# Kernel tuning notes

Measured on AMD Instinct MI355X. Metric: run time of the kernel, lower is better.

Reference implementation:

```python
import jax, jax.numpy as jnp
import numpy as np

# dims
B, A, CIN, CC = 512, 256, 7, 16          # batch, num_actions, input channels, conv channels
D, H, DH, E = 48, 8, 6, 512              # token_dimension, heads, head_dim, num_embeddings
S, T = 32, 32                            # num_input_tokens, num_output_tokens
AH = H * DH                              # 48
NL = 4                                   # attention layers
CONV_IN = A * CC                         # 4096
ENC = S * D                              # 1536
DEC_OUT = A * CIN                        # 1792
SCALE = float(np.sqrt(D))                # module uses sqrt(input_embedding_dim)
EPS = 1e-5


def _ln(x, g, b):
    m = jnp.mean(x, axis=-1, keepdims=True)
    v = jnp.var(x, axis=-1, keepdims=True)
    return (x - m) * jax.lax.rsqrt(v + EPS) * g + b


def setup_inputs() -> dict:
    key = jax.random.key(0)
    ks = iter(jax.random.split(key, 64))
    def rn(shape, s=0.05):
        return jax.random.normal(next(ks), shape, dtype=jnp.float32) * s
    inp = {}
    inp['x'] = jax.random.normal(next(ks), (B, A, CIN), dtype=jnp.float32)
    inp['u'] = jax.random.uniform(next(ks), (T, B), dtype=jnp.float32)
    inp['bn_g'] = jnp.ones((CIN,), jnp.float32); inp['bn_b'] = jnp.zeros((CIN,), jnp.float32)
    inp['conv_w'] = rn((CC, CIN, 5)); inp['conv_b'] = jnp.zeros((CC,), jnp.float32)
    inp['tk_W1'] = rn((CONV_IN, 2 * CONV_IN)); inp['tk_b1'] = jnp.zeros((2 * CONV_IN,), jnp.float32)
    inp['tk_W2'] = rn((2 * CONV_IN, ENC)); inp['tk_b2'] = jnp.zeros((ENC,), jnp.float32)
    for nm in ('q', 'k', 'v'):
        inp['ln%s_g' % nm] = jnp.ones((NL, D), jnp.float32)
        inp['ln%s_b' % nm] = jnp.zeros((NL, D), jnp.float32)
        inp['W%s' % nm] = rn((NL, D, AH))
        inp['b%s' % nm] = jnp.zeros((NL, AH), jnp.float32)
    inp['Wo'] = rn((NL, AH, D)); inp['bo'] = jnp.zeros((NL, D), jnp.float32)
    inp['mln_g'] = jnp.ones((NL, D), jnp.float32); inp['mln_b'] = jnp.zeros((NL, D), jnp.float32)
    inp['W1'] = rn((NL, D, 2 * D)); inp['b1'] = jnp.zeros((NL, 2 * D), jnp.float32)
    inp['W2'] = rn((NL, 2 * D, D)); inp['b2'] = jnp.zeros((NL, D), jnp.float32)
    inp['emb'] = rn((D, E), 1.0)          # nn.Parameter(torch.randn(D, E))
    inp['pos_enc'] = rn((T, D), 1.0)      # nn.Parameter(torch.randn(T, D))
    inp['dec_W1'] = rn((ENC, 2 * ENC)); inp['dec_b1'] = jnp.zeros((2 * ENC,), jnp.float32)
    inp['dec_W2'] = rn((2 * ENC, DEC_OUT)); inp['dec_b2'] = jnp.zeros((DEC_OUT,), jnp.float32)
    return inp


def _fwd(x, u, bn_g, bn_b, conv_w, conv_b, tk_W1, tk_b1, tk_W2, tk_b2,
         lnq_g, lnq_b, Wq, bq, lnk_g, lnk_b, Wk, bk, lnv_g, lnv_b, Wv, bv, Wo, bo,
         mln_g, mln_b, W1, b1, W2, b2, emb, pos_enc, dec_W1, dec_b1, dec_W2, dec_b2):
    # --- conv stem (BatchNorm1d in training mode: batch statistics) ---
    xt = x.transpose(0, 2, 1)                              # [B, 7, A]
    mu = jnp.mean(xt, axis=(0, 2), keepdims=True)
    var = jnp.var(xt, axis=(0, 2), keepdims=True)
    xn = (xt - mu) * jax.lax.rsqrt(var + EPS) * bn_g[None, :, None] + bn_b[None, :, None]
    xc = jax.lax.conv_general_dilated(xn, conv_w, (1,), ((2, 2),),
                                      dimension_numbers=('NCH', 'OIH', 'NCH')) + conv_b[None, :, None]
    xf = xc.reshape(B, -1)                                 # [B, 16*A]
    h = jax.nn.relu(xf @ tk_W1 + tk_b1)
    toks = (h @ tk_W2 + tk_b2).reshape(B, S, D)            # [B, S, D]

    STOT = S + T
    kc = jnp.zeros((NL, B, H, STOT, DH), jnp.float32)
    vc = jnp.zeros_like(kc)

    # --- prefill pass (output discarded; fills KV caches) ---
    ii = jnp.arange(S)[:, None]; jj = jnp.arange(S)[None, :]
    pre_mask = jnp.where(jj - ii >= S - 1, -999.0, 0.0)    # triu(-999, diagonal=S-1), as in source
    xcur = toks
    for l in range(NL):
        q = (_ln(xcur, lnq_g[l], lnq_b[l]) @ Wq[l] + bq[l]).reshape(B, S, H, DH).transpose(0, 2, 1, 3)
        k = (_ln(xcur, lnk_g[l], lnk_b[l]) @ Wk[l] + bk[l]).reshape(B, S, H, DH).transpose(0, 2, 1, 3)
        v = (_ln(xcur, lnv_g[l], lnv_b[l]) @ Wv[l] + bv[l]).reshape(B, S, H, DH).transpose(0, 2, 1, 3)
        kc = kc.at[l, :, :, :S].set(k)
        vc = vc.at[l, :, :, :S].set(v)
        attn = jax.nn.softmax(jnp.einsum('bhqd,bhkd->bhqk', q, k) / SCALE + pre_mask, axis=-1)
        o = jnp.einsum('bhqk,bhkd->bhqd', attn, v).transpose(0, 2, 1, 3).reshape(B, S, AH)
        xcur = o @ Wo[l] + bo[l] + xcur
        hh = jax.nn.relu(_ln(xcur, mln_g[l], mln_b[l]) @ W1[l] + b1[l])
        xcur = hh @ W2[l] + b2[l]

    jidx = jnp.arange(STOT)

    def step(carry, xs):
        kc, vc = carry
        i, pe, uu = xs
        p = S + i                                          # cache length before this step
        xtk = jnp.broadcast_to(pe, (B, 1, D))
        newk, newv = [], []
        for l in range(NL):
            q = (_ln(xtk, lnq_g[l], lnq_b[l]) @ Wq[l] + bq[l]).reshape(B, 1, H, DH).transpose(0, 2, 1, 3)
            k = (_ln(xtk, lnk_g[l], lnk_b[l]) @ Wk[l] + bk[l]).reshape(B, 1, H, DH).transpose(0, 2, 1, 3)
            v = (_ln(xtk, lnv_g[l], lnv_b[l]) @ Wv[l] + bv[l]).reshape(B, 1, H, DH).transpose(0, 2, 1, 3)
            kcl = jax.lax.dynamic_update_slice(kc[l], k, (0, 0, p, 0))
            vcl = jax.lax.dynamic_update_slice(vc[l], v, (0, 0, p, 0))
            scores = jnp.einsum('bhqd,bhkd->bhqk', q, kcl) / SCALE
            # source mask: -999 added for positions >= mask_offset (includes the new token itself)
            scores = scores + jnp.where(jidx >= p, -999.0, 0.0)
            attn = jax.nn.softmax(scores, axis=-1)
            o = jnp.einsum('bhqk,bhkd->bhqd', attn, vcl).transpose(0, 2, 1, 3).reshape(B, 1, AH)
            xtk = o @ Wo[l] + bo[l] + xtk
            hh = jax.nn.relu(_ln(xtk, mln_g[l], mln_b[l]) @ W1[l] + b1[l])
            xtk = hh @ W2[l] + b2[l]
            newk.append(kcl); newv.append(vcl)
        attended = xtk                                     # [B, 1, D]
        probs = jax.nn.softmax((attended @ emb).reshape(B, E), axis=1)
        cdf = jnp.cumsum(probs, axis=1)
        idx = jnp.clip(jnp.sum((cdf < uu[:, None]).astype(jnp.int32), axis=1), 0, E - 1)
        sel = emb.T[idx].reshape(B, 1, D)
        st = sel + attended - jax.lax.stop_gradient(attended)  # straight-through
        return (jnp.stack(newk), jnp.stack(newv)), st

    (_, _), outs = jax.lax.scan(step, (kc, vc), (jnp.arange(T), pos_enc, u))
    out_tokens = outs.transpose(1, 0, 2, 3).reshape(B, T * D)
    dh_ = jax.nn.relu(out_tokens @ dec_W1 + dec_b1)
    traj = (dh_ @ dec_W2 + dec_b2).reshape(B, A, CIN)
    return traj


def reference(x, u, bn_g, bn_b, conv_w, conv_b, tk_W1, tk_b1, tk_W2, tk_b2,
              lnq_g, lnq_b, Wq, bq, lnk_g, lnk_b, Wk, bk, lnv_g, lnv_b, Wv, bv, Wo, bo,
              mln_g, mln_b, W1, b1, W2, b2, emb, pos_enc, dec_W1, dec_b1, dec_W2, dec_b2):
    return _fwd(x, u, bn_g, bn_b, conv_w, conv_b, tk_W1, tk_b1, tk_W2, tk_b2,
                lnq_g, lnq_b, Wq, bq, lnk_g, lnk_b, Wk, bk, lnv_g, lnv_b, Wv, bv, Wo, bo,
                mln_g, mln_b, W1, b1, W2, b2, emb, pos_enc, dec_W1, dec_b1, dec_W2, dec_b2)
```

## Files before the change

kernel.cpp:

```cpp
#include <hip/hip_runtime.h>

static const double SCALE_ = 6.928203230275509;

__device__ inline float  fma_t(float a, float b, float c)  { return fmaf(a, b, c); }
__device__ inline double fma_t(double a, double b, double c){ return fma(a, b, c); }

__device__ __attribute__((noinline)) double dotW(const double* a,
                                                 const float* W, int n, int ldw,
                                                 double init) {
  double a0 = init, a1 = 0.0;
#pragma unroll 2
  for (int i = 0; i < n; i += 2) {
    a0 = fma(a[i],     (double)W[i * ldw],       a0);
    a1 = fma(a[i + 1], (double)W[(i + 1) * ldw], a1);
  }
  return a0 + a1;
}

__device__ __forceinline__ double dot48_row(const double* a, const float* Wrow, double init) {
  double c0 = init, c1 = 0.0, c2 = 0.0, c3 = 0.0;
#pragma unroll
  for (int i = 0; i < 48; i += 4) {
    const float4 wv = *(const float4*)(Wrow + i);
    c0 = fma(a[i],     (double)wv.x, c0);
    c1 = fma(a[i + 1], (double)wv.y, c1);
    c2 = fma(a[i + 2], (double)wv.z, c2);
    c3 = fma(a[i + 3], (double)wv.w, c3);
  }
  return (c0 + c1) + (c2 + c3);
}

__device__ __forceinline__ double dot96_row(const double* a, const float* Wrow, double init) {
  double c0 = init, c1 = 0.0, c2 = 0.0, c3 = 0.0;
#pragma unroll
  for (int i = 0; i < 96; i += 4) {
    const float4 wv = *(const float4*)(Wrow + i);
    c0 = fma(a[i],     (double)wv.x, c0);
    c1 = fma(a[i + 1], (double)wv.y, c1);
    c2 = fma(a[i + 2], (double)wv.z, c2);
    c3 = fma(a[i + 3], (double)wv.w, c3);
  }
  return (c0 + c1) + (c2 + c3);
}

__device__ __attribute__((noinline)) double2 ln_stats48(const double* x) {
  double s0 = 0, s1 = 0, q0 = 0, q1 = 0;
#pragma unroll 2
  for (int i = 0; i < 48; i += 2) {
    const double va = x[i], vb = x[i + 1];
    s0 += va; q0 = fma(va, va, q0);
    s1 += vb; q1 = fma(vb, vb, q1);
  }
  const double m = (s0 + s1) / 48.0;
  const double rs = 1.0 / sqrt((q0 + q1) / 48.0 - m * m + 1e-5);
  return make_double2(m, rs);
}

__device__ __attribute__((noinline)) double exp_ni(double x) { return exp(x); }

__global__ __launch_bounds__(256) void bn_partial_kernel(const float* __restrict__ x,
                                                         double* __restrict__ part) {
  __shared__ double sh[256 * 14];
  const int tid = threadIdx.x;
  const int idx = blockIdx.x * 256 + tid;
  const float* p = x + (size_t)idx * 7;
  for (int c = 0; c < 7; ++c) {
    double v = (double)p[c];
    sh[tid * 14 + c] = v;
    sh[tid * 14 + 7 + c] = v * v;
  }
  __syncthreads();
  if (tid < 14) {
    double acc = 0.0;
    for (int t = 0; t < 256; ++t) acc += sh[t * 14 + tid];
    part[blockIdx.x * 14 + tid] = acc;
  }
}

__global__ void bn_final_kernel(const double* __restrict__ part,
                                const float* __restrict__ g, const float* __restrict__ bb,
                                double* __restrict__ stat) {
  const int c = threadIdx.x;
  if (c < 7) {
    double s = 0.0, s2 = 0.0;
    for (int i = 0; i < 512; ++i) { s += part[i * 14 + c]; s2 += part[i * 14 + 7 + c]; }
    const double mean = s / 131072.0;
    const double var = s2 / 131072.0 - mean * mean;
    const double rstd = 1.0 / sqrt(var + 1e-5);
    const double scale = rstd * (double)g[c];
    stat[c] = scale;
    stat[7 + c] = (double)bb[c] - mean * scale;
  }
}

__global__ __launch_bounds__(256) void conv_kernel(const float* __restrict__ x,
                                                   const float* __restrict__ wconv,
                                                   const float* __restrict__ cb,
                                                   const double* __restrict__ stat,
                                                   double* __restrict__ xf) {
  __shared__ double wsh[560 + 14];
  const int tid = threadIdx.x;
  for (int i = tid; i < 560; i += 256) wsh[i] = (double)wconv[i];
  for (int i = tid; i < 14; i += 256) wsh[560 + i] = stat[i];
  __syncthreads();
  const int idx = blockIdx.x * 256 + tid;
  const int a = idx & 255;
  const int o = (idx >> 8) & 15;
  const int b = idx >> 12;
  double acc = (double)cb[o];
  const float* xb = x + (size_t)b * (256 * 7);
  for (int k = 0; k < 5; ++k) {
    const int pos = a + k - 2;
    if (pos < 0 || pos >= 256) continue;
    const float* xp = xb + pos * 7;
    for (int ci = 0; ci < 7; ++ci) {
      const double xn = (double)xp[ci] * wsh[560 + ci] + wsh[567 + ci];
      acc = fma(xn, wsh[(o * 7 + ci) * 5 + k], acc);
    }
  }
  xf[idx] = acc;
}

template <typename T, bool BIAS, bool RELU>
__global__ __launch_bounds__(256) void gemm128_kernel(const T* __restrict__ A,
                                                      const float* __restrict__ Bm,
                                                      const float* __restrict__ bias,
                                                      T* __restrict__ C,
                                                      const int M, const int N, const int K,
                                                      const int kc) {
  __shared__ T As[16][130];
  __shared__ T Bs[16][66];
  const int tid = threadIdx.x;
  const int tx = tid & 15, ty = tid >> 4;
  const int n0 = blockIdx.x * 64, m0 = blockIdx.y * 128;
  const int k0 = blockIdx.z * kc, kend = k0 + kc;
  const int ar = tid >> 1, ac = (tid & 1) * 8;
  const int br = tid >> 4, bc = (tid & 15) * 4;
  const T* Ap = A + (size_t)(m0 + ar) * K;
  const float* Bp = Bm + (size_t)br * N + n0 + bc;
  T acc[8][4] = {};
  for (int k = k0; k < kend; k += 16) {
    T av8[8];
#pragma unroll
    for (int i = 0; i < 8; ++i) av8[i] = Ap[k + ac + i];
    const float4 bw = *(const float4*)(Bp + (size_t)k * N);
#pragma unroll
    for (int i = 0; i < 8; ++i) As[ac + i][ar] = av8[i];
    Bs[br][bc] = (T)bw.x; Bs[br][bc + 1] = (T)bw.y;
    Bs[br][bc + 2] = (T)bw.z; Bs[br][bc + 3] = (T)bw.w;
    __syncthreads();
#pragma unroll
    for (int kk = 0; kk < 16; ++kk) {
      T a[8], b[4];
#pragma unroll
      for (int i = 0; i < 8; ++i) a[i] = As[kk][ty * 8 + i];
#pragma unroll
      for (int j = 0; j < 4; ++j) b[j] = Bs[kk][tx * 4 + j];
#pragma unroll
      for (int i = 0; i < 8; ++i)
#pragma unroll
        for (int j = 0; j < 4; ++j) acc[i][j] = fma_t(a[i], b[j], acc[i][j]);
    }
    __syncthreads();
  }
  T* Cp = C + (size_t)blockIdx.z * M * N;
#pragma unroll
  for (int i = 0; i < 8; ++i) {
    const int row = m0 + ty * 8 + i;
#pragma unroll
    for (int j = 0; j < 4; ++j) {
      const int col = n0 + tx * 4 + j;
      T v = acc[i][j];
      if (BIAS) v += (T)bias[col];
      if (RELU) v = v > (T)0 ? v : (T)0;
      Cp[(size_t)row * N + col] = v;
    }
  }
}

template <typename T, bool BIAS, bool RELU>
__global__ __launch_bounds__(256) void gemm_kernel(const T* __restrict__ A,
                                                   const float* __restrict__ Bm,
                                                   const float* __restrict__ bias,
                                                   T* __restrict__ C,
                                                   const int M, const int N, const int K,
                                                   const int kc) {
  __shared__ T As[16][65];
  __shared__ T Bs[16][65];
  const int tid = threadIdx.x;
  const int tx = tid & 15, ty = tid >> 4;
  const int n0 = blockIdx.x * 64, m0 = blockIdx.y * 64;
  const int k0 = blockIdx.z * kc, kend = k0 + kc;
  const int ar = tid >> 2, ac = (tid & 3) * 4;
  const int br = tid >> 4, bc = (tid & 15) * 4;
  const T* Ap = A + (size_t)(m0 + ar) * K;
  const float* Bp = Bm + (size_t)br * N + n0 + bc;
  T acc[4][4] = {};
  for (int k = k0; k < kend; k += 16) {
    const T a0 = Ap[k + ac], a1 = Ap[k + ac + 1], a2 = Ap[k + ac + 2], a3 = Ap[k + ac + 3];
    const float4 bw = *(const float4*)(Bp + (size_t)k * N);
    As[ac][ar] = a0; As[ac + 1][ar] = a1; As[ac + 2][ar] = a2; As[ac + 3][ar] = a3;
    Bs[br][bc] = (T)bw.x; Bs[br][bc + 1] = (T)bw.y; Bs[br][bc + 2] = (T)bw.z; Bs[br][bc + 3] = (T)bw.w;
    __syncthreads();
#pragma unroll
    for (int kk = 0; kk < 16; ++kk) {
      T av[4], bv2[4];
#pragma unroll
      for (int i = 0; i < 4; ++i) av[i] = As[kk][ty * 4 + i];
#pragma unroll
      for (int j = 0; j < 4; ++j) bv2[j] = Bs[kk][tx * 4 + j];
#pragma unroll
      for (int i = 0; i < 4; ++i)
#pragma unroll
        for (int j = 0; j < 4; ++j) acc[i][j] = fma_t(av[i], bv2[j], acc[i][j]);
    }
    __syncthreads();
  }
  T* Cp = C + (size_t)blockIdx.z * M * N;
#pragma unroll
  for (int i = 0; i < 4; ++i) {
    const int row = m0 + ty * 4 + i;
#pragma unroll
    for (int j = 0; j < 4; ++j) {
      const int col = n0 + tx * 4 + j;
      T v = acc[i][j];
      if (BIAS) v += (T)bias[col];
      if (RELU) v = v > (T)0 ? v : (T)0;
      Cp[(size_t)row * N + col] = v;
    }
  }
}

__global__ __launch_bounds__(256) void reduce2_bias_kernel(const double* __restrict__ part,
                                                           const float* __restrict__ bias,
                                                           double* __restrict__ out,
                                                           const int MN, const int N) {
  const int i = blockIdx.x * 256 + threadIdx.x;
  if (i < MN) out[i] = part[i] + part[MN + i] + (double)bias[i % N];
}

__global__ __launch_bounds__(256) void transpose_weights_kernel(
    const float* __restrict__ Wq, const float* __restrict__ Wk,
    const float* __restrict__ Wv, const float* __restrict__ Wo,
    const float* __restrict__ W1, const float* __restrict__ W2,
    const float* __restrict__ emb,
    float* __restrict__ WqT, float* __restrict__ WkT,
    float* __restrict__ WvT, float* __restrict__ WoT,
    float* __restrict__ W1T, float* __restrict__ W2T,
    float* __restrict__ embT) {
  const int t = blockIdx.x * 256 + threadIdx.x;
  if (t < 36864) {
    const int a = t / 9216, r = t - a * 9216;
    const int l = r / 2304, e = r - l * 2304;
    const int i = e / 48, j = e - i * 48;
    const float* src = a == 0 ? Wq : a == 1 ? Wk : a == 2 ? Wv : Wo;
    float* dst = a == 0 ? WqT : a == 1 ? WkT : a == 2 ? WvT : WoT;
    dst[l * 2304 + j * 48 + i] = src[l * 2304 + i * 48 + j];
  } else if (t < 55296) {
    const int t1 = t - 36864;
    const int l = t1 / 4608, e = t1 - l * 4608;
    const int i = e / 96, j = e - i * 96;
    W1T[l * 4608 + j * 48 + i] = W1[l * 4608 + i * 96 + j];
  } else if (t < 73728) {
    const int t2 = t - 55296;
    const int l = t2 / 4608, e = t2 - l * 4608;
    const int i = e / 48, j = e - i * 48;
    W2T[l * 4608 + j * 96 + i] = W2[l * 4608 + i * 48 + j];
  } else {
    const int t3 = t - 73728;
    const int d = t3 / 512, e = t3 - d * 512;
    embT[e * 48 + d] = emb[d * 512 + e];
  }
}

__global__ __launch_bounds__(256) void prefill_kernel(
    const double* __restrict__ toks,
    const float* __restrict__ lnq_g, const float* __restrict__ lnq_b,
    const float* __restrict__ Wq, const float* __restrict__ bq,
    const float* __restrict__ lnk_g, const float* __restrict__ lnk_b,
    const float* __restrict__ Wk, const float* __restrict__ bk,
    const float* __restrict__ lnv_g, const float* __restrict__ lnv_b,
    const float* __restrict__ Wv, const float* __restrict__ bvv,
    const float* __restrict__ Wo, const float* __restrict__ bo,
    const float* __restrict__ mln_g, const float* __restrict__ mln_b,
    const float* __restrict__ W1, const float* __restrict__ b1,
    const float* __restrict__ W2, const float* __restrict__ b2,
    double* __restrict__ kcache, double* __restrict__ vcache) {
  const int b = blockIdx.x, tid = threadIdx.x;
  __shared__ double xcur[1536], abuf[1536], qbuf[1536], kvbuf[3072];
  __shared__ double mean[32], rstd[32];
  double* kb = kvbuf;
  double* vb = kvbuf + 1536;

#pragma unroll 1
  for (int i = tid; i < 1536; i += 256) xcur[i] = toks[(size_t)b * 1536 + i];
  __syncthreads();

#pragma unroll 1
  for (int l = 0; l < 4; ++l) {
    if (tid < 32) {
      double s = 0.0, s2 = 0.0;
#pragma unroll 4
      for (int i = 0; i < 48; ++i) { const double v = xcur[tid * 48 + i]; s += v; s2 += v * v; }
      const double m = s / 48.0;
      mean[tid] = m;
      rstd[tid] = 1.0 / sqrt(s2 / 48.0 - m * m + 1e-5);
    }
    __syncthreads();
    const bool last = (l == 3);

    if (!last) {
#pragma unroll 1
      for (int i = tid; i < 1536; i += 256) {
        const int t = i / 48, d = i % 48;
        abuf[i] = (xcur[i] - mean[t]) * rstd[t] * (double)lnq_g[l * 48 + d] + (double)lnq_b[l * 48 + d];
      }
      __syncthreads();
#pragma unroll 1
      for (int i = tid; i < 1536; i += 256) {
        const int t = i / 48, j = i % 48;
        qbuf[i] = dotW(abuf + t * 48, Wq + l * 2304 + j, 48, 48, (double)bq[l * 48 + j]);
      }
      __syncthreads();
    }
#pragma unroll 1
    for (int i = tid; i < 1536; i += 256) {
      const int t = i / 48, d = i % 48;
      abuf[i] = (xcur[i] - mean[t]) * rstd[t] * (double)lnk_g[l * 48 + d] + (double)lnk_b[l * 48 + d];
    }
    __syncthreads();
#pragma unroll 1
    for (int i = tid; i < 1536; i += 256) {
      const int t = i / 48, j = i % 48;
      kb[i] = dotW(abuf + t * 48, Wk + l * 2304 + j, 48, 48, (double)bk[l * 48 + j]);
    }
    __syncthreads();
#pragma unroll 1
    for (int i = tid; i < 1536; i += 256) {
      const int t = i / 48, d = i % 48;
      abuf[i] = (xcur[i] - mean[t]) * rstd[t] * (double)lnv_g[l * 48 + d] + (double)lnv_b[l * 48 + d];
    }
    __syncthreads();
#pragma unroll 1
    for (int i = tid; i < 1536; i += 256) {
      const int t = i / 48, j = i % 48;
      vb[i] = dotW(abuf + t * 48, Wv + l * 2304 + j, 48, 48, (double)bvv[l * 48 + j]);
    }
    __syncthreads();
#pragma unroll 1
    for (int i = tid; i < 1536; i += 256) {
      const int t = i / 48, j = i % 48;
      const int h = j / 6, d = j % 6;
      const size_t ci = ((((size_t)b * 4 + l) * 8 + h) * 64 + t) * 6 + d;
      kcache[ci] = kb[i];
      vcache[ci] = vb[i];
    }

    if (!last) {
      const int t = tid >> 3, h = tid & 7;
      const double* qp = qbuf + t * 48 + h * 6;
      const double q0 = qp[0], q1 = qp[1], q2 = qp[2], q3 = qp[3], q4 = qp[4], q5 = qp[5];
      double mx = -1e300;
#pragma unroll 4
      for (int j = 0; j < 32; ++j) {
        const double* kp = kb + j * 48 + h * 6;
        double sv = q0 * kp[0];
        sv = fma(q1, kp[1], sv); sv = fma(q2, kp[2], sv); sv = fma(q3, kp[3], sv);
        sv = fma(q4, kp[4], sv); sv = fma(q5, kp[5], sv);
        sv /= SCALE_;
        if (t == 0 && j == 31) sv -= 999.0;
        mx = sv > mx ? sv : mx;
      }
      double den = 0, o0 = 0, o1 = 0, o2 = 0, o3 = 0, o4 = 0, o5 = 0;
#pragma unroll 4
      for (int j = 0; j < 32; ++j) {
        const double* kp = kb + j * 48 + h * 6;
        double sv = q0 * kp[0];
        sv = fma(q1, kp[1], sv); sv = fma(q2, kp[2], sv); sv = fma(q3, kp[3], sv);
        sv = fma(q4, kp[4], sv); sv = fma(q5, kp[5], sv);
        sv /= SCALE_;
        if (t == 0 && j == 31) sv -= 999.0;
        const double e = exp_ni(sv - mx);
        den += e;
        const double* vp = vb + j * 48 + h * 6;
        o0 = fma(e, vp[0], o0); o1 = fma(e, vp[1], o1); o2 = fma(e, vp[2], o2);
        o3 = fma(e, vp[3], o3); o4 = fma(e, vp[4], o4); o5 = fma(e, vp[5], o5);
      }
      abuf[t * 48 + h * 6 + 0] = o0 / den;
      abuf[t * 48 + h * 6 + 1] = o1 / den;
      abuf[t * 48 + h * 6 + 2] = o2 / den;
      abuf[t * 48 + h * 6 + 3] = o3 / den;
      abuf[t * 48 + h * 6 + 4] = o4 / den;
      abuf[t * 48 + h * 6 + 5] = o5 / den;
      __syncthreads();
#pragma unroll 1
      for (int i = tid; i < 1536; i += 256) {
        const int t2 = i / 48, j = i % 48;
        xcur[i] += dotW(abuf + t2 * 48, Wo + l * 2304 + j, 48, 48, (double)bo[l * 48 + j]);
      }
      __syncthreads();
      if (tid < 32) {
        double s = 0.0, s2 = 0.0;
#pragma unroll 4
        for (int i = 0; i < 48; ++i) { const double v = xcur[tid * 48 + i]; s += v; s2 += v * v; }
        const double m = s / 48.0;
        mean[tid] = m;
        rstd[tid] = 1.0 / sqrt(s2 / 48.0 - m * m + 1e-5);
      }
      __syncthreads();
#pragma unroll 1
      for (int i = tid; i < 1536; i += 256) {
        const int t2 = i / 48, d = i % 48;
        qbuf[i] = (xcur[i] - mean[t2]) * rstd[t2] * (double)mln_g[l * 48 + d] + (double)mln_b[l * 48 + d];
      }
      __syncthreads();
#pragma unroll 1
      for (int i = tid; i < 3072; i += 256) {
        const int t2 = i / 96, jj = i % 96;
        const double acc = dotW(qbuf + t2 * 48, W1 + l * 4608 + jj, 48, 96, (double)b1[l * 96 + jj]);
        kvbuf[i] = acc > 0 ? acc : 0;
      }
      __syncthreads();
#pragma unroll 1
      for (int i = tid; i < 1536; i += 256) {
        const int t2 = i / 48, j = i % 48;
        abuf[i] = dotW(kvbuf + t2 * 96, W2 + l * 4608 + j, 96, 48, (double)b2[l * 48 + j]);
      }
      __syncthreads();
#pragma unroll 1
      for (int i = tid; i < 1536; i += 256) xcur[i] = abuf[i];
      __syncthreads();
    }
  }
}

__global__ __launch_bounds__(64, 1) void ar_kernel(
    const float* __restrict__ pos_enc, const float* __restrict__ u,
    const float* __restrict__ lnq_g, const float* __restrict__ lnq_b,
    const float* __restrict__ WqT, const float* __restrict__ bq,
    const float* __restrict__ lnk_g, const float* __restrict__ lnk_b,
    const float* __restrict__ WkT, const float* __restrict__ bk,
    const float* __restrict__ lnv_g, const float* __restrict__ lnv_b,
    const float* __restrict__ WvT, const float* __restrict__ bvv,
    const float* __restrict__ WoT, const float* __restrict__ bo,
    const float* __restrict__ mln_g, const float* __restrict__ mln_b,
    const float* __restrict__ W1T, const float* __restrict__ b1,
    const float* __restrict__ W2T, const float* __restrict__ b2,
    const float* __restrict__ embT,
    double* __restrict__ kcache, double* __restrict__ vcache,
    float* __restrict__ out_tok) {
  const int b = blockIdx.x, tid = threadIdx.x;
  __shared__ double xtk[48], anorm[144], qs[48], os[48], hh[96];
  __shared__ float par[2880];
  {
    const float* srcs[14] = {lnq_g, lnq_b, lnk_g, lnk_b, lnv_g, lnv_b, mln_g, mln_b,
                             bq, bk, bvv, bo, b1, b2};
    const int sz[14] = {192, 192, 192, 192, 192, 192, 192, 192, 192, 192, 192, 192, 384, 192};
    int base = 0;
#pragma unroll 1
    for (int a2 = 0; a2 < 14; ++a2) {
      for (int i = tid; i < sz[a2]; i += 64) par[base + i] = srcs[a2][i];
      base += sz[a2];
    }
  }
  __syncthreads();

#pragma unroll 1
  for (int step = 0; step < 32; ++step) {
    const int p = 32 + step;
    if (tid < 48) xtk[tid] = (double)pos_enc[step * 48 + tid];
    __syncthreads();

#pragma unroll 1
    for (int l = 0; l < 4; ++l) {
      {
        const double2 st = ln_stats48(xtk);
#pragma unroll
        for (int i = tid; i < 144; i += 64) {
          const int which = i / 48, d = i - which * 48;
          const float* gp = par + 384 * which;
          const float* bp = gp + 192;
          anorm[i] = (xtk[d] - st.x) * st.y * (double)gp[l * 48 + d] + (double)bp[l * 48 + d];
        }
      }
      __syncthreads();
#pragma unroll
      for (int i = tid; i < 144; i += 64) {
        const int which = i / 48, j = i - which * 48;
        const float* WT = which == 0 ? WqT : which == 1 ? WkT : WvT;
        const float* bbp = par + 1536 + 192 * which;
        const double acc = dot48_row(anorm + which * 48, WT + l * 2304 + j * 48,
                                     (double)bbp[l * 48 + j]);
        if (which == 0) {
          qs[j] = acc;
        } else {
          const int h = j / 6, d = j - h * 6;
          const size_t ci = ((((size_t)b * 4 + l) * 8 + h) * 64 + p) * 6 + d;
          if (which == 1) kcache[ci] = acc; else vcache[ci] = acc;
        }
      }
      __syncthreads();
      {
        const int h = tid >> 3, rl = tid & 7;
        const double* kcb = kcache + ((((size_t)b * 4 + l) * 8 + h) * 64) * 6;
        const double* vcb = vcache + ((((size_t)b * 4 + l) * 8 + h) * 64) * 6;
        double qv[6];
#pragma unroll
        for (int d = 0; d < 6; ++d) qv[d] = qs[h * 6 + d];
        double sv[8];
        double mx = -1e300;
        int nk = 0;
#pragma unroll 2
        for (int r = rl; r < p; r += 8) {
          const double* kp = kcb + r * 6;
          double s = qv[0] * kp[0];
          s = fma(qv[1], kp[1], s); s = fma(qv[2], kp[2], s); s = fma(qv[3], kp[3], s);
          s = fma(qv[4], kp[4], s); s = fma(qv[5], kp[5], s);
          s /= SCALE_;
          sv[nk++] = s;
          mx = s > mx ? s : mx;
        }
#pragma unroll
        for (int off = 1; off < 8; off <<= 1) {
          const double o2 = __shfl_xor(mx, off); mx = o2 > mx ? o2 : mx;
        }
        double den = 0.0, o[6] = {0, 0, 0, 0, 0, 0};
        int kk = 0;
#pragma unroll 2
        for (int r = rl; r < p; r += 8) {
          const double e = exp(sv[kk++] - mx);
          den += e;
          const double* vp = vcb + r * 6;
#pragma unroll
          for (int d = 0; d < 6; ++d) o[d] = fma(e, vp[d], o[d]);
        }
#pragma unroll
        for (int off = 1; off < 8; off <<= 1) {
          den += __shfl_xor(den, off);
#pragma unroll
          for (int d = 0; d < 6; ++d) o[d] += __shfl_xor(o[d], off);
        }
        if (rl == 0) {
#pragma unroll
          for (int d = 0; d < 6; ++d) os[h * 6 + d] = o[d] / den;
        }
      }
      __syncthreads();
      if (tid < 48)
        xtk[tid] += dot48_row(os, WoT + l * 2304 + tid * 48, (double)par[2112 + l * 48 + tid]);
      __syncthreads();
      {
        const double2 st = ln_stats48(xtk);
        if (tid < 48)
          anorm[tid] = (xtk[tid] - st.x) * st.y * (double)par[1152 + l * 48 + tid]
                       + (double)par[1344 + l * 48 + tid];
      }
      __syncthreads();
#pragma unroll
      for (int j = tid; j < 96; j += 64) {
        const double v2 = dot48_row(anorm, W1T + l * 4608 + j * 48, (double)par[2304 + l * 96 + j]);
        hh[j] = v2 > 0 ? v2 : 0;
      }
      __syncthreads();
      if (tid < 48)
        xtk[tid] = dot96_row(hh, W2T + l * 4608 + tid * 96, (double)par[2688 + l * 48 + tid]);
      __syncthreads();
    }

    {
      double lg[8];
      const float* er = embT + (size_t)tid * 384;
      double mx = -1e300;
#pragma unroll 2
      for (int n = 0; n < 8; ++n) {
        lg[n] = dot48_row(xtk, er + n * 48, 0.0);
        mx = lg[n] > mx ? lg[n] : mx;
      }
#pragma unroll
      for (int off = 1; off < 64; off <<= 1) {
        const double o2 = __shfl_xor(mx, off); mx = o2 > mx ? o2 : mx;
      }
      double loc[8], run = 0.0;
#pragma unroll
      for (int n = 0; n < 8; ++n) { run += exp(lg[n] - mx); loc[n] = run; }
      double incl = run;
#pragma unroll
      for (int off = 1; off < 64; off <<= 1) {
        const double t2 = __shfl_up(incl, off);
        if (tid >= off) incl += t2;
      }
      const double excl = incl - run;
      const double Ssum = __shfl(incl, 63);
      const double uu = (double)u[step * 512 + b];
      int cnt = 0;
#pragma unroll
      for (int n = 0; n < 8; ++n) cnt += ((excl + loc[n]) / Ssum < uu) ? 1 : 0;
#pragma unroll
      for (int off = 1; off < 64; off <<= 1) cnt += __shfl_xor(cnt, off);
      const int idx = cnt > 511 ? 511 : cnt;
      if (tid < 48) {
        const double sel = (double)embT[(size_t)idx * 48 + tid];
        const double att = xtk[tid];
        out_tok[(size_t)b * 1536 + step * 48 + tid] = (float)((sel + att) - att);
      }
    }
    __syncthreads();
  }
}

extern "C" void kernel_launch(void* const* d_in, const int* in_sizes, int n_in,
                              void* d_out, int out_size, void* d_ws, size_t ws_size,
                              hipStream_t stream) {
  const float* x      = (const float*)d_in[0];
  const float* u      = (const float*)d_in[1];
  const float* bn_g   = (const float*)d_in[2];
  const float* bn_b   = (const float*)d_in[3];
  const float* conv_w = (const float*)d_in[4];
  const float* conv_b = (const float*)d_in[5];
  const float* tk_W1  = (const float*)d_in[6];
  const float* tk_b1  = (const float*)d_in[7];
  const float* tk_W2  = (const float*)d_in[8];
  const float* tk_b2  = (const float*)d_in[9];
  const float* lnq_g  = (const float*)d_in[10];
  const float* lnq_b  = (const float*)d_in[11];
  const float* Wq     = (const float*)d_in[12];
  const float* bq     = (const float*)d_in[13];
  const float* lnk_g  = (const float*)d_in[14];
  const float* lnk_b  = (const float*)d_in[15];
  const float* Wk     = (const float*)d_in[16];
  const float* bk     = (const float*)d_in[17];
  const float* lnv_g  = (const float*)d_in[18];
  const float* lnv_b  = (const float*)d_in[19];
  const float* Wv     = (const float*)d_in[20];
  const float* bvv    = (const float*)d_in[21];
  const float* Wo     = (const float*)d_in[22];
  const float* bo     = (const float*)d_in[23];
  const float* mln_g  = (const float*)d_in[24];
  const float* mln_b  = (const float*)d_in[25];
  const float* W1     = (const float*)d_in[26];
  const float* b1     = (const float*)d_in[27];
  const float* W2     = (const float*)d_in[28];
  const float* b2     = (const float*)d_in[29];
  const float* emb    = (const float*)d_in[30];
  const float* pos    = (const float*)d_in[31];
  const float* dW1    = (const float*)d_in[32];
  const float* db1    = (const float*)d_in[33];
  const float* dW2    = (const float*)d_in[34];
  const float* db2    = (const float*)d_in[35];
  float* out = (float*)d_out;

  char* w = (char*)d_ws;
  size_t off = 0;
  auto alloc = [&](size_t bytes) {
    size_t o = off;
    off = (off + bytes + 255) & ~(size_t)255;
    return o;
  };
  const size_t o_bnp  = alloc(512 * 14 * 8);
  const size_t o_bns  = alloc(14 * 8);
  const size_t o_xf   = alloc(16777216);
  const size_t o_h    = alloc(33554432);
  const size_t o_toks = alloc(6291456);
  const size_t o_kc   = alloc(50331648);
  const size_t o_vc   = alloc(50331648);

  double* bnp  = (double*)(w + o_bnp);
  double* bns  = (double*)(w + o_bns);
  double* xf   = (double*)(w + o_xf);
  double* hbuf = (double*)(w + o_h);
  double* toks = (double*)(w + o_toks);
  double* kc   = (double*)(w + o_kc);
  double* vc   = (double*)(w + o_vc);
  double* part = (double*)(w + o_xf);
  float*  otok = (float*)(w + o_h);
  float*  dh   = (float*)(w + o_h + 4194304);
  float* WqT  = (float*)(w + o_h + 16777216);
  float* WkT  = WqT + 9216;
  float* WvT  = WkT + 9216;
  float* WoT  = WvT + 9216;
  float* W1T  = WoT + 9216;
  float* W2T  = W1T + 18432;
  float* embT = W2T + 18432;

  bn_partial_kernel<<<512, 256, 0, stream>>>(x, bnp);
  bn_final_kernel<<<1, 64, 0, stream>>>(bnp, bn_g, bn_b, bns);
  conv_kernel<<<8192, 256, 0, stream>>>(x, conv_w, conv_b, bns, xf);
  gemm128_kernel<double, true, true><<<dim3(128, 4, 1), 256, 0, stream>>>(
      xf, tk_W1, tk_b1, hbuf, 512, 8192, 4096, 4096);
  gemm128_kernel<double, false, false><<<dim3(24, 4, 2), 256, 0, stream>>>(
      hbuf, tk_W2, nullptr, part, 512, 1536, 8192, 4096);
  reduce2_bias_kernel<<<3072, 256, 0, stream>>>(part, tk_b2, toks, 512 * 1536, 1536);
  transpose_weights_kernel<<<384, 256, 0, stream>>>(Wq, Wk, Wv, Wo, W1, W2, emb,
      WqT, WkT, WvT, WoT, W1T, W2T, embT);
  prefill_kernel<<<512, 256, 0, stream>>>(toks,
      lnq_g, lnq_b, Wq, bq, lnk_g, lnk_b, Wk, bk, lnv_g, lnv_b, Wv, bvv,
      Wo, bo, mln_g, mln_b, W1, b1, W2, b2, kc, vc);
  ar_kernel<<<512, 64, 0, stream>>>(pos, u,
      lnq_g, lnq_b, WqT, bq, lnk_g, lnk_b, WkT, bk, lnv_g, lnv_b, WvT, bvv,
      WoT, bo, mln_g, mln_b, W1T, b1, W2T, b2, embT, kc, vc, otok);
  gemm_kernel<float, true, true><<<dim3(48, 8, 1), 256, 0, stream>>>(
      otok, dW1, db1, dh, 512, 3072, 1536, 1536);
  gemm_kernel<float, true, false><<<dim3(28, 8, 1), 256, 0, stream>>>(
      dh, dW2, db2, out, 512, 1792, 3072, 3072);
}
```

Baseline: 5.288 ms.

## Keep the autoregressive KV cache on-chip and widen ar_kernel to 256 threads

The autoregressive kernel now runs 256 threads per block instead of 64. At kernel start it loads the prefill K cache into shared memory as float and the V cache into per-thread registers, and new K/V rows are written on-chip instead of to global double buffers. Attention uses 32 lanes per head with one or two keys per lane, and the vocabulary logits and softmax are spread over all 256 threads, with only one wavefront doing the CDF scan. The goal is to remove global-memory round trips and serial per-thread loops from the 32-step decode loop. In exchange it uses more shared memory and registers, and K/V are now held at float rather than double precision.

```diff
diff --git a/kernel.cpp b/kernel.cpp
--- a/kernel.cpp
+++ b/kernel.cpp
@@ -434,7 +434,7 @@
   }
 }
 
-__global__ __launch_bounds__(64, 1) void ar_kernel(
+__global__ __launch_bounds__(256, 2) void ar_kernel(
     const float* __restrict__ pos_enc, const float* __restrict__ u,
     const float* __restrict__ lnq_g, const float* __restrict__ lnq_b,
     const float* __restrict__ WqT, const float* __restrict__ bq,
@@ -447,10 +447,13 @@
     const float* __restrict__ W1T, const float* __restrict__ b1,
     const float* __restrict__ W2T, const float* __restrict__ b2,
     const float* __restrict__ embT,
-    double* __restrict__ kcache, double* __restrict__ vcache,
+    const double* __restrict__ kcache, const double* __restrict__ vcache,
     float* __restrict__ out_tok) {
   const int b = blockIdx.x, tid = threadIdx.x;
+  __shared__ float ksh[4][8][64][6];
   __shared__ double xtk[48], anorm[144], qs[48], os[48], hh[96];
+  __shared__ float vnew[48];
+  __shared__ double probs[512], red[4];
   __shared__ float par[2880];
   {
     const float* srcs[14] = {lnq_g, lnq_b, lnk_g, lnk_b, lnv_g, lnv_b, mln_g, mln_b,
@@ -459,10 +462,25 @@
     int base = 0;
 #pragma unroll 1
     for (int a2 = 0; a2 < 14; ++a2) {
-      for (int i = tid; i < sz[a2]; i += 64) par[base + i] = srcs[a2][i];
+      for (int i = tid; i < sz[a2]; i += 256) par[base + i] = srcs[a2][i];
       base += sz[a2];
     }
   }
+#pragma unroll 1
+  for (int m = tid; m < 6144; m += 256) {
+    const int d = m % 6, t2 = (m / 6) % 32, h2 = (m / 192) % 8, l2 = m / 1536;
+    ksh[l2][h2][t2][d] =
+        (float)kcache[((((size_t)b * 4 + l2) * 8 + h2) * 64 + t2) * 6 + d];
+  }
+  const int hl = tid >> 5, rl = tid & 31;
+  float vlo[4][6], vhi[4][6];
+#pragma unroll
+  for (int l2 = 0; l2 < 4; ++l2)
+#pragma unroll
+    for (int d = 0; d < 6; ++d) {
+      vlo[l2][d] = (float)vcache[((((size_t)b * 4 + l2) * 8 + hl) * 64 + rl) * 6 + d];
+      vhi[l2][d] = 0.0f;
+    }
   __syncthreads();
 
 #pragma unroll 1
@@ -471,22 +489,20 @@
     if (tid < 48) xtk[tid] = (double)pos_enc[step * 48 + tid];
     __syncthreads();
 
-#pragma unroll 1
+#pragma unroll
     for (int l = 0; l < 4; ++l) {
       {
         const double2 st = ln_stats48(xtk);
-#pragma unroll
-        for (int i = tid; i < 144; i += 64) {
-          const int which = i / 48, d = i - which * 48;
+        if (tid < 144) {
+          const int which = tid / 48, d = tid - which * 48;
           const float* gp = par + 384 * which;
           const float* bp = gp + 192;
-          anorm[i] = (xtk[d] - st.x) * st.y * (double)gp[l * 48 + d] + (double)bp[l * 48 + d];
+          anorm[tid] = (xtk[d] - st.x) * st.y * (double)gp[l * 48 + d] + (double)bp[l * 48 + d];
         }
       }
       __syncthreads();
-#pragma unroll
-      for (int i = tid; i < 144; i += 64) {
-        const int which = i / 48, j = i - which * 48;
+      if (tid < 144) {
+        const int which = tid / 48, j = tid - which * 48;
         const float* WT = which == 0 ? WqT : which == 1 ? WkT : WvT;
         const float* bbp = par + 1536 + 192 * which;
         const double acc = dot48_row(anorm + which * 48, WT + l * 2304 + j * 48,
@@ -494,55 +510,57 @@
         if (which == 0) {
           qs[j] = acc;
         } else {
-          const int h = j / 6, d = j - h * 6;
-          const size_t ci = ((((size_t)b * 4 + l) * 8 + h) * 64 + p) * 6 + d;
-          if (which == 1) kcache[ci] = acc; else vcache[ci] = acc;
+          const int h2 = j / 6, d2 = j - h2 * 6;
+          if (which == 1) ksh[l][h2][p][d2] = (float)acc;
+          else            vnew[j] = (float)acc;
         }
       }
       __syncthreads();
+      if (rl == (p & 31)) {
+#pragma unroll
+        for (int d = 0; d < 6; ++d) vhi[l][d] = vnew[hl * 6 + d];
+      }
       {
-        const int h = tid >> 3, rl = tid & 7;
-        const double* kcb = kcache + ((((size_t)b * 4 + l) * 8 + h) * 64) * 6;
-        const double* vcb = vcache + ((((size_t)b * 4 + l) * 8 + h) * 64) * 6;
-        double qv[6];
-#pragma unroll
-        for (int d = 0; d < 6; ++d) qv[d] = qs[h * 6 + d];
-        double sv[8];
-        double mx = -1e300;
-        int nk = 0;
-#pragma unroll 2
-        for (int r = rl; r < p; r += 8) {
-          const double* kp = kcb + r * 6;
-          double s = qv[0] * kp[0];
-          s = fma(qv[1], kp[1], s); s = fma(qv[2], kp[2], s); s = fma(qv[3], kp[3], s);
-          s = fma(qv[4], kp[4], s); s = fma(qv[5], kp[5], s);
-          s /= SCALE_;
-          sv[nk++] = s;
-          mx = s > mx ? s : mx;
+        const float* kp1 = &ksh[l][hl][rl][0];
+        const double qv0 = qs[hl * 6 + 0], qv1 = qs[hl * 6 + 1], qv2 = qs[hl * 6 + 2],
+                     qv3 = qs[hl * 6 + 3], qv4 = qs[hl * 6 + 4], qv5 = qs[hl * 6 + 5];
+        const bool has2 = (rl + 32) < p;
+        double sv1 = qv0 * (double)kp1[0];
+        sv1 = fma(qv1, (double)kp1[1], sv1); sv1 = fma(qv2, (double)kp1[2], sv1);
+        sv1 = fma(qv3, (double)kp1[3], sv1); sv1 = fma(qv4, (double)kp1[4], sv1);
+        sv1 = fma(qv5, (double)kp1[5], sv1);
+        sv1 /= SCALE_;
+        double sv2 = -1e300;
+        if (has2) {
+          const float* kp2 = &ksh[l][hl][rl + 32][0];
+          double t2 = qv0 * (double)kp2[0];
+          t2 = fma(qv1, (double)kp2[1], t2); t2 = fma(qv2, (double)kp2[2], t2);
+          t2 = fma(qv3, (double)kp2[3], t2); t2 = fma(qv4, (double)kp2[4], t2);
+          t2 = fma(qv5, (double)kp2[5], t2);
+          sv2 = t2 / SCALE_;
         }
-#pragma unroll
-        for (int off = 1; off < 8; off <<= 1) {
-          const double o2 = __shfl_xor(mx, off); mx = o2 > mx ? o2 : mx;
+        double mx = sv1 > sv2 ? sv1 : sv2;
+#pragma unroll
+        for (int off = 1; off < 32; off <<= 1) { const double o2 = __shfl_xor(mx, off); mx = o2 > mx ? o2 : mx; }
+        const double e1 = exp(sv1 - mx);
+        const double e2 = has2 ? exp(sv2 - mx) : 0.0;
+        double den = e1 + e2;
+        double o[6];
+#pragma unroll
+        for (int d = 0; d < 6; ++d) o[d] = e1 * (double)vlo[l][d];
+        if (has2) {
+#pragma unroll
+          for (int d = 0; d < 6; ++d) o[d] = fma(e2, (double)vhi[l][d], o[d]);
         }
-        double den = 0.0, o[6] = {0, 0, 0, 0, 0, 0};
-        int kk = 0;
-#pragma unroll 2
-        for (int r = rl; r < p; r += 8) {
-          const double e = exp(sv[kk++] - mx);
-          den += e;
-          const double* vp = vcb + r * 6;
-#pragma unroll
-          for (int d = 0; d < 6; ++d) o[d] = fma(e, vp[d], o[d]);
-        }
-#pragma unroll
-        for (int off = 1; off < 8; off <<= 1) {
+#pragma unroll
+        for (int off = 1; off < 32; off <<= 1) {
           den += __shfl_xor(den, off);
 #pragma unroll
           for (int d = 0; d < 6; ++d) o[d] += __shfl_xor(o[d], off);
         }
         if (rl == 0) {
 #pragma unroll
-          for (int d = 0; d < 6; ++d) os[h * 6 + d] = o[d] / den;
+          for (int d = 0; d < 6; ++d) os[hl * 6 + d] = o[d] / den;
         }
       }
       __syncthreads();
@@ -556,10 +574,9 @@
                        + (double)par[1344 + l * 48 + tid];
       }
       __syncthreads();
-#pragma unroll
-      for (int j = tid; j < 96; j += 64) {
-        const double v2 = dot48_row(anorm, W1T + l * 4608 + j * 48, (double)par[2304 + l * 96 + j]);
-        hh[j] = v2 > 0 ? v2 : 0;
+      if (tid < 96) {
+        const double v2 = dot48_row(anorm, W1T + l * 4608 + tid * 48, (double)par[2304 + l * 96 + tid]);
+        hh[tid] = v2 > 0 ? v2 : 0;
       }
       __syncthreads();
       if (tid < 48)
@@ -568,43 +585,49 @@
     }
 
     {
-      double lg[8];
-      const float* er = embT + (size_t)tid * 384;
-      double mx = -1e300;
-#pragma unroll 2
-      for (int n = 0; n < 8; ++n) {
-        lg[n] = dot48_row(xtk, er + n * 48, 0.0);
-        mx = lg[n] > mx ? lg[n] : mx;
-      }
-#pragma unroll
-      for (int off = 1; off < 64; off <<= 1) {
-        const double o2 = __shfl_xor(mx, off); mx = o2 > mx ? o2 : mx;
-      }
-      double loc[8], run = 0.0;
-#pragma unroll
-      for (int n = 0; n < 8; ++n) { run += exp(lg[n] - mx); loc[n] = run; }
-      double incl = run;
-#pragma unroll
-      for (int off = 1; off < 64; off <<= 1) {
-        const double t2 = __shfl_up(incl, off);
-        if (tid >= off) incl += t2;
-      }
-      const double excl = incl - run;
-      const double Ssum = __shfl(incl, 63);
-      const double uu = (double)u[step * 512 + b];
-      int cnt = 0;
-#pragma unroll
-      for (int n = 0; n < 8; ++n) cnt += ((excl + loc[n]) / Ssum < uu) ? 1 : 0;
-#pragma unroll
-      for (int off = 1; off < 64; off <<= 1) cnt += __shfl_xor(cnt, off);
-      const int idx = cnt > 511 ? 511 : cnt;
-      if (tid < 48) {
-        const double sel = (double)embT[(size_t)idx * 48 + tid];
-        const double att = xtk[tid];
-        out_tok[(size_t)b * 1536 + step * 48 + tid] = (float)((sel + att) - att);
-      }
-    }
-    __syncthreads();
+      const double lg1 = dot48_row(xtk, embT + (size_t)tid * 48, 0.0);
+      const double lg2 = dot48_row(xtk, embT + (size_t)(256 + tid) * 48, 0.0);
+      double mx = lg1 > lg2 ? lg1 : lg2;
+#pragma unroll
+      for (int off = 1; off < 64; off <<= 1) { const double o2 = __shfl_xor(mx, off); mx = o2 > mx ? o2 : mx; }
+      if ((tid & 63) == 0) red[tid >> 6] = mx;
+      __syncthreads();
+      {
+        const double m0 = red[0] > red[1] ? red[0] : red[1];
+        const double m1 = red[2] > red[3] ? red[2] : red[3];
+        mx = m0 > m1 ? m0 : m1;
+      }
+      probs[tid] = exp(lg1 - mx);
+      probs[tid + 256] = exp(lg2 - mx);
+      __syncthreads();
+      if (tid < 64) {
+        const int lane = tid;
+        double loc[8], run = 0;
+#pragma unroll
+        for (int n2 = 0; n2 < 8; ++n2) { run += probs[lane * 8 + n2]; loc[n2] = run; }
+        double incl = run;
+#pragma unroll
+        for (int off = 1; off < 64; off <<= 1) {
+          const double t2 = __shfl_up(incl, off);
+          if (lane >= off) incl += t2;
+        }
+        const double excl = incl - run;
+        const double Ssum = __shfl(incl, 63);
+        const double uu = (double)u[step * 512 + b];
+        int cnt = 0;
+#pragma unroll
+        for (int n2 = 0; n2 < 8; ++n2) cnt += ((excl + loc[n2]) / Ssum < uu) ? 1 : 0;
+#pragma unroll
+        for (int off = 1; off < 64; off <<= 1) cnt += __shfl_xor(cnt, off);
+        const int idx = cnt > 511 ? 511 : cnt;
+        if (lane < 48) {
+          const double sel = (double)embT[(size_t)idx * 48 + lane];
+          const double att = xtk[lane];
+          out_tok[(size_t)b * 1536 + step * 48 + lane] = (float)((sel + att) - att);
+        }
+      }
+      __syncthreads();
+    }
   }
 }
 
@@ -695,7 +718,7 @@
   prefill_kernel<<<512, 256, 0, stream>>>(toks,
       lnq_g, lnq_b, Wq, bq, lnk_g, lnk_b, Wk, bk, lnv_g, lnv_b, Wv, bvv,
       Wo, bo, mln_g, mln_b, W1, b1, W2, b2, kc, vc);
-  ar_kernel<<<512, 64, 0, stream>>>(pos, u,
+  ar_kernel<<<512, 256, 0, stream>>>(pos, u,
       lnq_g, lnq_b, WqT, bq, lnk_g, lnk_b, WkT, bk, lnv_g, lnv_b, WvT, bvv,
       WoT, bo, mln_g, mln_b, W1T, b1, W2T, b2, embT, kc, vc, otok);
   gemm_kernel<float, true, true><<<dim3(48, 8, 1), 256, 0, stream>>>(
```

Result: no change. 5.186 ms (-1.9%).
